# Kernel optimization log

Measured on AMD Instinct MI355X. Metric: run time of the kernel, lower is better.

## Reference

```python
import jax, jax.numpy as jnp
import numpy as np
from jax import lax

B, T, F_DIM, E, H, L = 128, 160, 512, 64, 1024, 2
IN0 = F_DIM + E  # LSTM layer-0 input size (feat + target embedding)


def setup_inputs() -> dict:
    key = jax.random.key(0)
    ks = jax.random.split(key, 20)
    s_in0 = 1.0 / np.sqrt(IN0)
    s_h = 1.0 / np.sqrt(H)
    inp = {
        "feat": jax.random.normal(ks[0], (B, T, F_DIM), jnp.float32),
        "embedded_labels": jax.random.normal(ks[1], (B, T, E), jnp.float32),
        "mask": jax.random.bernoulli(ks[2], 0.3, (B, T)),
        # LSTM layer 0 (input IN0 -> H), gate order i,f,g,o as in torch
        "W_ih0": jax.random.normal(ks[3], (4 * H, IN0), jnp.float32) * s_in0,
        "W_hh0": jax.random.normal(ks[4], (4 * H, H), jnp.float32) * s_h,
        "b_ih0": jax.random.normal(ks[5], (4 * H,), jnp.float32) * s_h,
        "b_hh0": jax.random.normal(ks[6], (4 * H,), jnp.float32) * s_h,
        # LSTM layer 1 (H -> H)
        "W_ih1": jax.random.normal(ks[7], (4 * H, H), jnp.float32) * s_h,
        "W_hh1": jax.random.normal(ks[8], (4 * H, H), jnp.float32) * s_h,
        "b_ih1": jax.random.normal(ks[9], (4 * H,), jnp.float32) * s_h,
        "b_hh1": jax.random.normal(ks[10], (4 * H,), jnp.float32) * s_h,
        # target embedding: mu [B,1] @ W_tgt [1,E] + b_tgt
        "W_tgt": jax.random.normal(ks[11], (1, E), jnp.float32),
        "b_tgt": jax.random.normal(ks[12], (E,), jnp.float32) * 0.1,
        # mu / sigma projections from flattened hidden [B, H*L]
        "mu_w": jax.random.normal(ks[13], (H * L, 1), jnp.float32) * (1.0 / np.sqrt(H * L)),
        "mu_b": jnp.zeros((1,), jnp.float32),
        "sig_w": jax.random.normal(ks[14], (H * L, 1), jnp.float32) * (1.0 / np.sqrt(H * L)),
        "sig_b": jnp.zeros((1,), jnp.float32),
    }
    return inp


def _lstm_cell(x, h, c, W_ih, W_hh, b_ih, b_hh):
    g = x @ W_ih.T + b_ih + h @ W_hh.T + b_hh  # [B, 4H]
    gi, gf, gg, go = jnp.split(g, 4, axis=-1)
    c = jax.nn.sigmoid(gf) * c + jax.nn.sigmoid(gi) * jnp.tanh(gg)
    h = jax.nn.sigmoid(go) * jnp.tanh(c)
    return h, c


def reference(feat, embedded_labels, mask,
              W_ih0, W_hh0, b_ih0, b_hh0,
              W_ih1, W_hh1, b_ih1, b_hh1,
              W_tgt, b_tgt, mu_w, mu_b, sig_w, sig_b):
    Bq, Tq, _ = feat.shape
    Hq = W_hh0.shape[1]

    def step(carry, xs):
        h0, c0, h1, c1, mu = carry
        x_t, lab_t, m_t, idx = xs
        mu_embed = mu @ W_tgt + b_tgt  # [B, E]
        # i==0 always uses embedded_labels; otherwise where(mask, mu_embed, label)
        use_mu = (idx > 0) & m_t[:, None]
        lab = jnp.where(use_mu, mu_embed, lab_t)
        x = jnp.concatenate([x_t, lab], axis=-1)  # [B, IN0]
        h0, c0 = _lstm_cell(x, h0, c0, W_ih0, W_hh0, b_ih0, b_hh0)
        h1, c1 = _lstm_cell(h0, h1, c1, W_ih1, W_hh1, b_ih1, b_hh1)
        # torch: hidden[0].permute(1,2,0).view(B, H*L)
        hp = jnp.stack([h0, h1], axis=0).transpose(1, 2, 0).reshape(Bq, -1)
        mu = hp @ mu_w + mu_b  # [B, 1]
        sig = jax.nn.softplus(hp @ sig_w + sig_b)  # [B, 1]
        return (h0, c0, h1, c1, mu), (mu[:, 0], sig[:, 0])

    z = jnp.zeros((Bq, Hq), feat.dtype)
    init = (z, z, z, z, jnp.zeros((Bq, 1), feat.dtype))
    xs = (feat.transpose(1, 0, 2), embedded_labels.transpose(1, 0, 2),
          mask.T, jnp.arange(Tq))
    _, (mus, sigs) = lax.scan(step, init, xs)
    # [T,B] -> [B,T]; DeepAR stacks (mu, sigma) on last axis
    return jnp.stack((mus.T, sigs.T), axis=-1)  # [B, T, 2]
```

## Files before the change

kernel.cpp:

```cpp
#include <hip/hip_runtime.h>


#define B_   128
#define T_   160
#define FD   512
#define E_   64
#define H_   1024
#define NT   512
#define NBLK 256
#define CH0  100
#define CH1  128
#define HT_ELEMS (64 * 4 * 512)

typedef unsigned short u16;
typedef unsigned long long u64;
typedef __attribute__((ext_vector_type(8))) short bf16x8;
typedef __attribute__((ext_vector_type(16))) float f32x16;

__device__ __forceinline__ bf16x8 ld8(const u16* p) {
    return *reinterpret_cast<const bf16x8*>(p);
}
__device__ __forceinline__ float4 ld4f(const float* p) {
    u64* q = (u64*)p;
    union { u64 v[2]; float4 f; } u_;
    u_.v[0] = __hip_atomic_load(q + 0, __ATOMIC_RELAXED, __HIP_MEMORY_SCOPE_AGENT);
    u_.v[1] = __hip_atomic_load(q + 1, __ATOMIC_RELAXED, __HIP_MEMORY_SCOPE_AGENT);
    return u_.f;
}
__device__ __forceinline__ f32x16 mfma32(bf16x8 a, bf16x8 b, f32x16 c) {
    return __builtin_amdgcn_mfma_f32_32x32x16_bf16(a, b, c, 0, 0, 0);
}
__device__ __forceinline__ u16 f2bf(float x) {
    unsigned u = __float_as_uint(x);
    u += 0x7FFFu + ((u >> 16) & 1u);
    return (u16)(u >> 16);
}
__device__ __forceinline__ float sigm(float x)  { return 1.f / (1.f + __expf(-x)); }
__device__ __forceinline__ float tanh_(float x) { return 1.f - 2.f / (__expf(2.f * x) + 1.f); }
__device__ __forceinline__ float softp(float x) { return x > 20.f ? x : log1pf(__expf(x)); }

__device__ __forceinline__ void st_u32(unsigned* p, unsigned v) {
    __hip_atomic_store(p, v, __ATOMIC_RELAXED, __HIP_MEMORY_SCOPE_AGENT);
}
__device__ __forceinline__ void st_f32(float* p, float v) {
    __hip_atomic_store(p, v, __ATOMIC_RELAXED, __HIP_MEMORY_SCOPE_AGENT);
}


__device__ __forceinline__ void wait_rel(unsigned* rel, unsigned tgt, bool acq) {
    if (threadIdx.x == 0) {
        while (__hip_atomic_load(rel, __ATOMIC_RELAXED, __HIP_MEMORY_SCOPE_AGENT) < tgt)
            __builtin_amdgcn_s_sleep(2);
        if (acq)
            (void)__hip_atomic_load(rel, __ATOMIC_ACQUIRE, __HIP_MEMORY_SCOPE_AGENT);
    }
    __atomic_signal_fence(__ATOMIC_ACQUIRE);
    __syncthreads();
}
__device__ __forceinline__ void arrive_release(unsigned* cnt, unsigned* rel) {
    __builtin_amdgcn_s_waitcnt(0);
    __syncthreads();
    if (threadIdx.x == 0) {
        unsigned n = __hip_atomic_fetch_add(cnt, 1u, __ATOMIC_RELAXED,
                                            __HIP_MEMORY_SCOPE_AGENT) + 1u;
        if ((n & 127u) == 0u)
            __hip_atomic_store(rel, n >> 7, __ATOMIC_RELAXED,
                               __HIP_MEMORY_SCOPE_AGENT);
    }
}


__global__ void detect_mask(const unsigned* __restrict__ m, int* __restrict__ flags) {
    int i = blockIdx.x * 256 + threadIdx.x;
    unsigned w = m[i];
    if (w > 1u) atomicOr(&flags[0], 1);
    if (w != 0u && w != 0x3F800000u) atomicOr(&flags[1], 1);
}

__global__ void featconv(const float* __restrict__ feat, u16* __restrict__ fb2) {
    int i = blockIdx.x * 256 + threadIdx.x;
    int t = i >> 14;
    int u = i & 16383;
    int c = u >> 9;
    int r = u & 511;
    int mm = r >> 7;
    int l  = (r >> 1) & 63;
    int jj = r & 1;
    int b = mm * 32 + (l & 31);
    int k = c * 16 + (l >> 5) * 8 + jj * 4;
    float4 v = reinterpret_cast<const float4*>(feat)[((size_t)b * T_ + t) * 128 + (k >> 2)];
    ushort4 o = make_ushort4(f2bf(v.x), f2bf(v.y), f2bf(v.z), f2bf(v.w));
    reinterpret_cast<ushort4*>(fb2)[((((size_t)t * 32 + c) * 4 + mm) * 512 + l * 8 + jj * 4) >> 2] = o;
}


struct SM0 {
    u16   bw[CH0 * 512];
    float gtb[4224];
    float mu_s[128];
    float uu[32], vv[32], bias[32];
    float mwv[8], swv[8];
    unsigned char msk[128];
};
struct SM1 {
    u16   bw[CH1 * 512];
    float gtb[4224];
    float bias[32];
    float mwv[8], swv[8];
};
union SMU { SM0 a; SM1 b; };

__global__ void __launch_bounds__(NT, 2) persist(
    const u16* __restrict__ fb2, const float* __restrict__ emb,
    const void* __restrict__ mask, const int* __restrict__ flags,
    const float* __restrict__ Wih0, const float* __restrict__ Whh0,
    const float* __restrict__ bih0, const float* __restrict__ bhh0,
    const float* __restrict__ Wih1, const float* __restrict__ Whh1,
    const float* __restrict__ bih1, const float* __restrict__ bhh1,
    const float* __restrict__ Wtgt, const float* __restrict__ btgt,
    const float* __restrict__ muw, const float* __restrict__ mubp,
    const float* __restrict__ sgw, const float* __restrict__ sgbp,
    u16* __restrict__ h0T, u16* __restrict__ h1T,
    float* __restrict__ muacc, float* __restrict__ sgacc,
    unsigned* __restrict__ actr,
    float* __restrict__ out)
{
    __shared__ SMU smu;
    const int tid  = threadIdx.x;
    const int blk  = blockIdx.x;
    const bool isL0 = blk < 128;
    const int g    = isL0 ? blk : blk - 128;
    const int wv   = tid >> 6;
    const int m    = wv & 3;
    const int s    = wv >> 2;
    const int lane = tid & 63;
    const int l31  = lane & 31;

    unsigned* f0c  = actr;
    unsigned* f1c  = actr + 32;
    unsigned* rel0 = actr + 64;
    unsigned* rel1 = actr + 96;

    const float mub_r = mubp[0], sgb_r = sgbp[0];

    if (isL0) {
        SM0& s0 = smu.a;
        for (int i = tid; i < CH0 * 512; i += NT) {
            int ch = i >> 9, r = i & 511, l = r >> 3, jj = r & 7;
            int pc = l & 31;
            int kk = ch * 16 + (l >> 5) * 8 + jj;
            int q = pc & 3, j = pc >> 2;
            int row = q * H_ + g * 8 + j;
            float v = (kk < 576) ? Wih0[row * 576 + kk]
                                 : Whh0[(size_t)row * H_ + (kk - 576)];
            s0.bw[i] = f2bf(v);
        }
        if (tid < 32) {
            int pc = tid, q = pc & 3, j = pc >> 2;
            int row = q * H_ + g * 8 + j;
            s0.bias[pc] = bih0[row] + bhh0[row];
            float su = 0.f, sv = 0.f;
            for (int e = 0; e < 64; ++e) {
                float wl = Wih0[row * 576 + 512 + e];
                su += Wtgt[e] * wl;
                sv += btgt[e] * wl;
            }
            s0.uu[pc] = su; s0.vv[pc] = sv;
        }
        if (tid < 8) {
            int h = g * 8 + tid;
            s0.mwv[tid] = muw[2 * h]; s0.swv[tid] = sgw[2 * h];
        }
    } else {
        SM1& s1 = smu.b;
        for (int i = tid; i < CH1 * 512; i += NT) {
            int ch = i >> 9, r = i & 511, l = r >> 3, jj = r & 7;
            int pc = l & 31;
            int kk = ch * 16 + (l >> 5) * 8 + jj;
            int q = pc & 3, j = pc >> 2;
            int row = q * H_ + g * 8 + j;
            float v = (kk < 1024) ? Wih1[(size_t)row * H_ + kk]
                                  : Whh1[(size_t)row * H_ + (kk - 1024)];
            s1.bw[i] = f2bf(v);
        }
        if (tid < 32) {
            int pc = tid, q = pc & 3, j = pc >> 2;
            int row = q * H_ + g * 8 + j;
            s1.bias[pc] = bih1[row] + bhh1[row];
        }
        if (tid < 8) {
            int h = g * 8 + tid;
            s1.mwv[tid] = muw[2 * h + 1]; s1.swv[tid] = sgw[2 * h + 1];
        }
    }
    const int nonbin = flags[0], nonfl = flags[1];
    __syncthreads();

    float creg0 = 0.f, creg1 = 0.f;
    f32x16 acc;
    #pragma unroll
    for (int r = 0; r < 16; ++r) acc[r] = 0.f;

    auto reduce_gates = [&](float* g_) {
        if (s == 1) {
            #pragma unroll
            for (int r = 0; r < 16; ++r) g_[r * 256 + m * 64 + lane] = acc[r];
        }
        __syncthreads();
        f32x16 tot;
        if (s == 0) {
            #pragma unroll
            for (int r = 0; r < 16; ++r) tot[r] = acc[r] + g_[r * 256 + m * 64 + lane];
        }
        __syncthreads();
        if (s == 0) {
            #pragma unroll
            for (int r = 0; r < 16; ++r) {
                int row = m * 32 + (r & 3) + 8 * (r >> 2) + 4 * (lane >> 5);
                g_[row * 33 + l31] = tot[r];
            }
        }
        #pragma unroll
        for (int r = 0; r < 16; ++r) acc[r] = 0.f;
    };

    auto hgemm = [&](const u16* hp, const u16* bwb) {
        bf16x8 areg[32];
        #pragma unroll
        for (int c = 0; c < 32; ++c) {
            int ch = s * 32 + c;
            areg[c] = ld8(hp + ((size_t)ch * 4 + m) * 512 + lane * 8);
        }
        #pragma unroll
        for (int c = 0; c < 32; ++c) {
            int ch = s * 32 + c;
            bf16x8 b = *(const bf16x8*)&bwb[ch * 512 + lane * 8];
            acc = mfma32(areg[c], b, acc);
        }
    };

    auto featlab = [&](int t1, bool use_mask) {
        SM0& s0 = smu.a;
        const int bq = m * 32 + l31;
        bool um = false;
        if (use_mask && s == 1) {
            int mi = bq * T_ + t1;
            um = !nonbin ? (reinterpret_cast<const int*>(mask)[mi] != 0)
               : !nonfl  ? (reinterpret_cast<const float*>(mask)[mi] != 0.f)
                         : (reinterpret_cast<const unsigned char*>(mask)[mi] != 0);
        }
        #pragma unroll 6
        for (int c = 0; c < 18; ++c) {
            int ch = s * 18 + c;
            bf16x8 a;
            if (ch < 32) {
                a = ld8(fb2 + (((size_t)t1 * 32 + ch) * 4 + m) * 512 + lane * 8);
            } else {
                const float* ep = &emb[((size_t)bq * T_ + t1) * 64
                                       + (ch - 32) * 16 + (lane >> 5) * 8];
                float4 v0 = *reinterpret_cast<const float4*>(ep);
                float4 v1 = *reinterpret_cast<const float4*>(ep + 4);
                if (um) { v0.x=v0.y=v0.z=v0.w=0.f; v1.x=v1.y=v1.z=v1.w=0.f; }
                a[0] = (short)f2bf(v0.x); a[1] = (short)f2bf(v0.y);
                a[2] = (short)f2bf(v0.z); a[3] = (short)f2bf(v0.w);
                a[4] = (short)f2bf(v1.x); a[5] = (short)f2bf(v1.y);
                a[6] = (short)f2bf(v1.z); a[7] = (short)f2bf(v1.w);
            }
            bf16x8 b = *(const bf16x8*)&s0.bw[ch * 512 + lane * 8];
            acc = mfma32(a, b, acc);
        }
    };

    if (isL0) {
        featlab(0, false);
        reduce_gates(smu.a.gtb);
    }

    for (int t = 0; t < T_; ++t) {
        const int pcur = t & 1, pprev = pcur ^ 1;

        if (isL0) {
            SM0& s0 = smu.a;
            if (t > 0) {
                wait_rel(rel1, (unsigned)t, false);
                if (tid < 128) {
                    float4 x = ld4f(&muacc[(pprev * 128 + tid) * 8]);
                    float4 y = ld4f(&muacc[(pprev * 128 + tid) * 8 + 4]);
                    s0.mu_s[tid] = (x.x + x.y) + (x.z + x.w) + (y.x + y.y) + (y.z + y.w) + mub_r;
                    int mi = tid * T_ + t;
                    bool um = !nonbin ? (reinterpret_cast<const int*>(mask)[mi] != 0)
                            : !nonfl  ? (reinterpret_cast<const float*>(mask)[mi] != 0.f)
                                      : (reinterpret_cast<const unsigned char*>(mask)[mi] != 0);
                    s0.msk[tid] = um ? 1 : 0;
                }
            }
            __syncthreads();
            if (t > 0 && tid == 0) {
                float4 x = ld4f(&sgacc[(pprev * 128 + g) * 8]);
                float4 y = ld4f(&sgacc[(pprev * 128 + g) * 8 + 4]);
                float sg = (x.x + x.y) + (x.z + x.w) + (y.x + y.y) + (y.z + y.w) + sgb_r;
                out[((size_t)g * T_ + (t - 1)) * 2 + 0] = s0.mu_s[g];
                out[((size_t)g * T_ + (t - 1)) * 2 + 1] = softp(sg);
            }
            u16* hw = h0T + (size_t)pcur * HT_ELEMS;
            const int c_ = g >> 1, half = g & 1;
            #pragma unroll
            for (int p = 0; p < 2; ++p) {
                int id = tid + p * NT;
                int b = id >> 3, j = id & 7;
                float gi = s0.gtb[b * 33 + 4 * j + 0] + s0.bias[4 * j + 0];
                float gf = s0.gtb[b * 33 + 4 * j + 1] + s0.bias[4 * j + 1];
                float gg = s0.gtb[b * 33 + 4 * j + 2] + s0.bias[4 * j + 2];
                float go = s0.gtb[b * 33 + 4 * j + 3] + s0.bias[4 * j + 3];
                if (t > 0 && s0.msk[b]) {
                    float mu = s0.mu_s[b];
                    gi += mu * s0.uu[4 * j + 0] + s0.vv[4 * j + 0];
                    gf += mu * s0.uu[4 * j + 1] + s0.vv[4 * j + 1];
                    gg += mu * s0.uu[4 * j + 2] + s0.vv[4 * j + 2];
                    go += mu * s0.uu[4 * j + 3] + s0.vv[4 * j + 3];
                }
                float cold = (p == 0) ? creg0 : creg1;
                float cn = sigm(gf) * cold + sigm(gi) * tanh_(gg);
                float hn = sigm(go) * tanh_(cn);
                if (p == 0) creg0 = cn; else creg1 = cn;
                unsigned hv = f2bf(hn);
                unsigned other = (unsigned)__shfl_xor((int)hv, 1);
                if ((j & 1) == 0) {
                    int l = half * 32 + (b & 31), mb = b >> 5;
                    st_u32(reinterpret_cast<unsigned*>(hw + ((size_t)(c_ * 4 + mb) * 512 + l * 8 + j)),
                           hv | (other << 16));
                }
                float pmu = hn * s0.mwv[j], psg = hn * s0.swv[j];
                pmu += __shfl_xor(pmu, 1); pmu += __shfl_xor(pmu, 2); pmu += __shfl_xor(pmu, 4);
                psg += __shfl_xor(psg, 1); psg += __shfl_xor(psg, 2); psg += __shfl_xor(psg, 4);
                if (j == 0) {
                    atomicAdd(&muacc[(pcur * 128 + b) * 8 + (g & 7)], pmu);
                    atomicAdd(&sgacc[(pcur * 128 + b) * 8 + (g & 7)], psg);
                }
            }
            arrive_release(f0c, rel0);

            if (t + 1 < T_) {
                wait_rel(rel0, (unsigned)(t + 1), true);
                hgemm(h0T + (size_t)pcur * HT_ELEMS, &s0.bw[36 * 512]);
                featlab(t + 1, true);
                reduce_gates(s0.gtb);
            }
        } else {
            SM1& s1 = smu.b;
            if (t > 0) {
                wait_rel(rel1, (unsigned)t, true);
                hgemm(h1T + (size_t)pprev * HT_ELEMS, &s1.bw[64 * 512]);
            }
            wait_rel(rel0, (unsigned)(t + 1), true);
            if (t > 0 && tid < 8) {
                st_f32(&muacc[(pprev * 128 + g) * 8 + tid], 0.f);
                st_f32(&sgacc[(pprev * 128 + g) * 8 + tid], 0.f);
            }
            hgemm(h0T + (size_t)pcur * HT_ELEMS, &s1.bw[0]);
            reduce_gates(s1.gtb);
            __syncthreads();
            u16* hw = h1T + (size_t)pcur * HT_ELEMS;
            const int c_ = g >> 1, half = g & 1;
            #pragma unroll
            for (int p = 0; p < 2; ++p) {
                int id = tid + p * NT;
                int b = id >> 3, j = id & 7;
                float gi = s1.gtb[b * 33 + 4 * j + 0] + s1.bias[4 * j + 0];
                float gf = s1.gtb[b * 33 + 4 * j + 1] + s1.bias[4 * j + 1];
                float gg = s1.gtb[b * 33 + 4 * j + 2] + s1.bias[4 * j + 2];
                float go = s1.gtb[b * 33 + 4 * j + 3] + s1.bias[4 * j + 3];
                float cold = (p == 0) ? creg0 : creg1;
                float cn = sigm(gf) * cold + sigm(gi) * tanh_(gg);
                float hn = sigm(go) * tanh_(cn);
                if (p == 0) creg0 = cn; else creg1 = cn;
                unsigned hv = f2bf(hn);
                unsigned other = (unsigned)__shfl_xor((int)hv, 1);
                if ((j & 1) == 0) {
                    int l = half * 32 + (b & 31), mb = b >> 5;
                    st_u32(reinterpret_cast<unsigned*>(hw + ((size_t)(c_ * 4 + mb) * 512 + l * 8 + j)),
                           hv | (other << 16));
                }
                float pmu = hn * s1.mwv[j], psg = hn * s1.swv[j];
                pmu += __shfl_xor(pmu, 1); pmu += __shfl_xor(pmu, 2); pmu += __shfl_xor(pmu, 4);
                psg += __shfl_xor(psg, 1); psg += __shfl_xor(psg, 2); psg += __shfl_xor(psg, 4);
                if (j == 0) {
                    atomicAdd(&muacc[(pcur * 128 + b) * 8 + (g & 7)], pmu);
                    atomicAdd(&sgacc[(pcur * 128 + b) * 8 + (g & 7)], psg);
                }
            }
            arrive_release(f1c, rel1);
        }
    }

    if (isL0) {
        wait_rel(rel1, (unsigned)T_, false);
        if (tid == 0) {
            float4 x = ld4f(&muacc[(1 * 128 + g) * 8]);
            float4 y = ld4f(&muacc[(1 * 128 + g) * 8 + 4]);
            float mu = (x.x + x.y) + (x.z + x.w) + (y.x + y.y) + (y.z + y.w) + mub_r;
            float4 z = ld4f(&sgacc[(1 * 128 + g) * 8]);
            float4 u2 = ld4f(&sgacc[(1 * 128 + g) * 8 + 4]);
            float sg = (z.x + z.y) + (z.z + z.w) + (u2.x + u2.y) + (u2.z + u2.w) + sgb_r;
            out[((size_t)g * T_ + (T_ - 1)) * 2 + 0] = mu;
            out[((size_t)g * T_ + (T_ - 1)) * 2 + 1] = softp(sg);
        }
    }
}


extern "C" void kernel_launch(void* const* d_in, const int* in_sizes, int n_in,
                              void* d_out, int out_size, void* d_ws, size_t ws_size,
                              hipStream_t stream) {
    const float* feat = (const float*)d_in[0];
    const float* emb  = (const float*)d_in[1];
    const void*  mask = d_in[2];
    const float* Wih0 = (const float*)d_in[3];
    const float* Whh0 = (const float*)d_in[4];
    const float* bih0 = (const float*)d_in[5];
    const float* bhh0 = (const float*)d_in[6];
    const float* Wih1 = (const float*)d_in[7];
    const float* Whh1 = (const float*)d_in[8];
    const float* bih1 = (const float*)d_in[9];
    const float* bhh1 = (const float*)d_in[10];
    const float* Wtgt = (const float*)d_in[11];
    const float* btgt = (const float*)d_in[12];
    const float* muw  = (const float*)d_in[13];
    const float* mub  = (const float*)d_in[14];
    const float* sgw  = (const float*)d_in[15];
    const float* sgb  = (const float*)d_in[16];
    float* out = (float*)d_out;
    char* ws = (char*)d_ws;
    (void)in_sizes; (void)n_in; (void)out_size; (void)ws_size;

    size_t off = 0;
    auto alloc = [&](size_t bytes) {
        size_t o = off;
        off = (off + bytes + 255) & ~(size_t)255;
        return o;
    };
    size_t o_flags = alloc(256);
    size_t o_actr  = alloc(4 * 32 * 4);
    size_t o_muacc = alloc((size_t)2 * 128 * 8 * 4);
    size_t o_sgacc = alloc((size_t)2 * 128 * 8 * 4);
    size_t zero_end = off;
    size_t o_h0    = alloc((size_t)2 * HT_ELEMS * 2);
    size_t o_h1    = alloc((size_t)2 * HT_ELEMS * 2);
    size_t o_fb2   = alloc((size_t)T_ * 32 * 4 * 512 * 2);

    int*      flags = (int*)(ws + o_flags);
    unsigned* actr  = (unsigned*)(ws + o_actr);
    float*    muacc = (float*)(ws + o_muacc);
    float*    sgacc = (float*)(ws + o_sgacc);
    u16*      h0    = (u16*)(ws + o_h0);
    u16*      h1    = (u16*)(ws + o_h1);
    u16*      fb2   = (u16*)(ws + o_fb2);

    hipMemsetAsync(ws, 0, zero_end, stream);
    detect_mask<<<20, 256, 0, stream>>>((const unsigned*)mask, flags);
    featconv<<<10240, 256, 0, stream>>>(feat, fb2);

    persist<<<NBLK, NT, 0, stream>>>(
        fb2, emb, mask, flags,
        Wih0, Whh0, bih0, bhh0,
        Wih1, Whh1, bih1, bhh1,
        Wtgt, btgt, muw, mub, sgw, sgb,
        h0, h1, muacc, sgacc, actr, out);
}
```

Baseline: 3.282 ms.

## Split h-ready and mu/sigma-ready barriers to release hidden state earlier

Each layer's cell update now signals a first counter as soon as its bf16 hidden state is stored, before doing the mu/sigma partial-sum shuffles and atomics. A second counter per layer marks completion of those atomics, and layer 0 waits on both second counters before reading mu for the next step. The aim is to let the dependent GEMM in the next stage start earlier, taking the projection reduction off the critical path. The cost is extra atomic counters and one more barrier per step.

```diff
diff --git a/kernel.cpp b/kernel.cpp
--- a/kernel.cpp
+++ b/kernel.cpp
@@ -53,6 +53,16 @@
             __builtin_amdgcn_s_sleep(2);
         if (acq)
             (void)__hip_atomic_load(rel, __ATOMIC_ACQUIRE, __HIP_MEMORY_SCOPE_AGENT);
+    }
+    __atomic_signal_fence(__ATOMIC_ACQUIRE);
+    __syncthreads();
+}
+__device__ __forceinline__ void wait_two(unsigned* ra, unsigned* rb, unsigned tgt) {
+    if (threadIdx.x == 0) {
+        while (__hip_atomic_load(ra, __ATOMIC_RELAXED, __HIP_MEMORY_SCOPE_AGENT) < tgt)
+            __builtin_amdgcn_s_sleep(2);
+        while (__hip_atomic_load(rb, __ATOMIC_RELAXED, __HIP_MEMORY_SCOPE_AGENT) < tgt)
+            __builtin_amdgcn_s_sleep(2);
     }
     __atomic_signal_fence(__ATOMIC_ACQUIRE);
     __syncthreads();
@@ -136,10 +146,14 @@
     const int lane = tid & 63;
     const int l31  = lane & 31;
 
-    unsigned* f0c  = actr;
-    unsigned* f1c  = actr + 32;
-    unsigned* rel0 = actr + 64;
-    unsigned* rel1 = actr + 96;
+    unsigned* f0c   = actr;
+    unsigned* f1c   = actr + 32;
+    unsigned* f0b   = actr + 64;
+    unsigned* f1b   = actr + 96;
+    unsigned* rel0  = actr + 128;
+    unsigned* rel1  = actr + 160;
+    unsigned* rel0b = actr + 192;
+    unsigned* rel1b = actr + 224;
 
     const float mub_r = mubp[0], sgb_r = sgbp[0];
 
@@ -282,7 +296,7 @@
         if (isL0) {
             SM0& s0 = smu.a;
             if (t > 0) {
-                wait_rel(rel1, (unsigned)t, false);
+                wait_two(rel0b, rel1b, (unsigned)t);
                 if (tid < 128) {
                     float4 x = ld4f(&muacc[(pprev * 128 + tid) * 8]);
                     float4 y = ld4f(&muacc[(pprev * 128 + tid) * 8 + 4]);
@@ -302,6 +316,7 @@
                 out[((size_t)g * T_ + (t - 1)) * 2 + 0] = s0.mu_s[g];
                 out[((size_t)g * T_ + (t - 1)) * 2 + 1] = softp(sg);
             }
+            float hn_st0 = 0.f, hn_st1 = 0.f;
             u16* hw = h0T + (size_t)pcur * HT_ELEMS;
             const int c_ = g >> 1, half = g & 1;
             #pragma unroll
@@ -322,7 +337,8 @@
                 float cold = (p == 0) ? creg0 : creg1;
                 float cn = sigm(gf) * cold + sigm(gi) * tanh_(gg);
                 float hn = sigm(go) * tanh_(cn);
-                if (p == 0) creg0 = cn; else creg1 = cn;
+                if (p == 0) { creg0 = cn; hn_st0 = hn; }
+                else        { creg1 = cn; hn_st1 = hn; }
                 unsigned hv = f2bf(hn);
                 unsigned other = (unsigned)__shfl_xor((int)hv, 1);
                 if ((j & 1) == 0) {
@@ -330,6 +346,14 @@
                     st_u32(reinterpret_cast<unsigned*>(hw + ((size_t)(c_ * 4 + mb) * 512 + l * 8 + j)),
                            hv | (other << 16));
                 }
+            }
+            arrive_release(f0c, rel0);
+
+            #pragma unroll
+            for (int p = 0; p < 2; ++p) {
+                int id = tid + p * NT;
+                int b = id >> 3, j = id & 7;
+                float hn = (p == 0) ? hn_st0 : hn_st1;
                 float pmu = hn * s0.mwv[j], psg = hn * s0.swv[j];
                 pmu += __shfl_xor(pmu, 1); pmu += __shfl_xor(pmu, 2); pmu += __shfl_xor(pmu, 4);
                 psg += __shfl_xor(psg, 1); psg += __shfl_xor(psg, 2); psg += __shfl_xor(psg, 4);
@@ -338,7 +362,7 @@
                     atomicAdd(&sgacc[(pcur * 128 + b) * 8 + (g & 7)], psg);
                 }
             }
-            arrive_release(f0c, rel0);
+            arrive_release(f0b, rel0b);
 
             if (t + 1 < T_) {
                 wait_rel(rel0, (unsigned)(t + 1), true);
@@ -360,6 +384,7 @@
             hgemm(h0T + (size_t)pcur * HT_ELEMS, &s1.bw[0]);
             reduce_gates(s1.gtb);
             __syncthreads();
+            float hn_st0 = 0.f, hn_st1 = 0.f;
             u16* hw = h1T + (size_t)pcur * HT_ELEMS;
             const int c_ = g >> 1, half = g & 1;
             #pragma unroll
@@ -373,7 +398,8 @@
                 float cold = (p == 0) ? creg0 : creg1;
                 float cn = sigm(gf) * cold + sigm(gi) * tanh_(gg);
                 float hn = sigm(go) * tanh_(cn);
-                if (p == 0) creg0 = cn; else creg1 = cn;
+                if (p == 0) { creg0 = cn; hn_st0 = hn; }
+                else        { creg1 = cn; hn_st1 = hn; }
                 unsigned hv = f2bf(hn);
                 unsigned other = (unsigned)__shfl_xor((int)hv, 1);
                 if ((j & 1) == 0) {
@@ -381,6 +407,14 @@
                     st_u32(reinterpret_cast<unsigned*>(hw + ((size_t)(c_ * 4 + mb) * 512 + l * 8 + j)),
                            hv | (other << 16));
                 }
+            }
+            arrive_release(f1c, rel1);
+
+            #pragma unroll
+            for (int p = 0; p < 2; ++p) {
+                int id = tid + p * NT;
+                int b = id >> 3, j = id & 7;
+                float hn = (p == 0) ? hn_st0 : hn_st1;
                 float pmu = hn * s1.mwv[j], psg = hn * s1.swv[j];
                 pmu += __shfl_xor(pmu, 1); pmu += __shfl_xor(pmu, 2); pmu += __shfl_xor(pmu, 4);
                 psg += __shfl_xor(psg, 1); psg += __shfl_xor(psg, 2); psg += __shfl_xor(psg, 4);
@@ -389,12 +423,12 @@
                     atomicAdd(&sgacc[(pcur * 128 + b) * 8 + (g & 7)], psg);
                 }
             }
-            arrive_release(f1c, rel1);
+            arrive_release(f1b, rel1b);
         }
     }
 
     if (isL0) {
-        wait_rel(rel1, (unsigned)T_, false);
+        wait_two(rel0b, rel1b, (unsigned)T_);
         if (tid == 0) {
             float4 x = ld4f(&muacc[(1 * 128 + g) * 8]);
             float4 y = ld4f(&muacc[(1 * 128 + g) * 8 + 4]);
@@ -440,7 +474,7 @@
         return o;
     };
     size_t o_flags = alloc(256);
-    size_t o_actr  = alloc(4 * 32 * 4);
+    size_t o_actr  = alloc(8 * 32 * 4);
     size_t o_muacc = alloc((size_t)2 * 128 * 8 * 4);
     size_t o_sgacc = alloc((size_t)2 * 128 * 8 * 4);
     size_t zero_end = off;
```

New measurement: 3.061 ms. 6.7% less time.
